# Performance work log

Hardware: AMD Instinct MI355X
Metric: run time of the kernel (lower is better)

The kernel has to match this reference:

```python
import jax, jax.numpy as jnp
import numpy as np

H = 2048
Q_RANK = 256
SCALE = float(np.sqrt(Q_RANK))


def setup_inputs() -> dict:
    key = jax.random.key(0)
    k_x, k_s, k_a, k_o, k_b = jax.random.split(key, 5)
    B, L = 4, 4096
    x = jax.random.normal(k_x, (B, L, H), dtype=jnp.float32)
    # nn.Linear(H, q_rank, bias=False): weight [q_rank, H]; y = x @ W.T -> store transposed [H, q_rank]
    Ws = jax.random.normal(k_s, (H, Q_RANK), dtype=jnp.float32) / np.sqrt(H)
    Wa = jax.random.normal(k_a, (H, Q_RANK), dtype=jnp.float32) / np.sqrt(H)
    Wo = jax.random.normal(k_o, (H, H), dtype=jnp.float32) / np.sqrt(H)
    bo = jax.random.normal(k_b, (H,), dtype=jnp.float32) * 0.01
    return {"x": x, "Ws": Ws, "Wa": Wa, "Wo": Wo, "bo": bo}


def reference(x, Ws, Wa, Wo, bo):
    # x: [B, L, H]
    B, L, _ = x.shape
    state = jnp.einsum('blh,hr->blr', x, Ws)   # [B, L, r]
    action = jnp.einsum('blh,hr->blr', x, Wa)  # [B, L, r]
    q_values = jnp.einsum('bir,bjr->bij', state, action) / SCALE  # [B, L, L]
    # causal mask: position i attends to j <= i
    causal = jnp.tril(jnp.ones((L, L), dtype=bool))
    q_values = jnp.where(causal, q_values, -jnp.inf)
    weights = jax.nn.softmax(q_values, axis=-1)  # [B, L, L]
    out = jnp.einsum('bij,bjh->bih', weights, x)  # weights @ x (x acts as V)
    return jnp.einsum('bih,ho->bio', out, Wo.T) + bo  # out_proj: y = out @ Wo_lin.T; Wo stored as [H,H] input-major
```

## Files before the change

kernel.cpp:

```cpp
#include <hip/hip_runtime.h>
#include <hip/hip_bf16.h>
#include <cstdint>
#include <cstddef>

typedef __bf16 bf16_t;
typedef __bf16 bf16x8 __attribute__((ext_vector_type(8)));
typedef __bf16 bf16x4v __attribute__((ext_vector_type(4)));
typedef float f32x4 __attribute__((ext_vector_type(4)));

#define B_SZ 4
#define L_SZ 4096
#define H_SZ 2048
#define R_SZ 256
#define EXP_SC 0.090168440f
#define E2_ELEMS 8912896L
#define E2_BYTES 17825792L

#define GLDS16(gaddr, laddr)                                                    \
  __builtin_amdgcn_global_load_lds(                                             \
      (const __attribute__((address_space(1))) void*)(gaddr),                   \
      (__attribute__((address_space(3))) void*)(laddr), 16, 0, 0)

__device__ __forceinline__ f32x4 mfma16(bf16x8 a, bf16x8 b, f32x4 c) {
  return __builtin_amdgcn_mfma_f32_16x16x32_bf16(a, b, c, 0, 0, 0);
}

__device__ __forceinline__ float rsum16(float v) {
  v += __shfl_xor(v, 1, 16);
  v += __shfl_xor(v, 2, 16);
  v += __shfl_xor(v, 4, 16);
  v += __shfl_xor(v, 8, 16);
  return v;
}

__global__ void cvt_x_kernel(const float* __restrict__ x, bf16_t* __restrict__ xb, int n4) {
  int i = blockIdx.x * blockDim.x + threadIdx.x;
  const int stride = gridDim.x * blockDim.x;
  for (; i < n4; i += stride) {
    float4 v = reinterpret_cast<const float4*>(x)[i];
    bf16x4v o;
    o[0] = (bf16_t)v.x; o[1] = (bf16_t)v.y; o[2] = (bf16_t)v.z; o[3] = (bf16_t)v.w;
    reinterpret_cast<bf16x4v*>(xb)[i] = o;
  }
}

__global__ void cvt_w_kernel(const float* __restrict__ Ws, const float* __restrict__ Wa,
                             const float* __restrict__ Wo,
                             bf16_t* __restrict__ Wst, bf16_t* __restrict__ Wat,
                             bf16_t* __restrict__ Wob, float* __restrict__ lsum) {
  const int tid = blockIdx.x * blockDim.x + threadIdx.x;
  const int stride = gridDim.x * blockDim.x;
  for (int idx = tid; idx < R_SZ * H_SZ; idx += stride) {
    const int rr = idx >> 11;
    const int h  = idx & (H_SZ - 1);
    Wst[idx] = (bf16_t)Ws[h * R_SZ + rr];
    Wat[idx] = (bf16_t)Wa[h * R_SZ + rr];
  }
  for (int idx = tid; idx < H_SZ * H_SZ; idx += stride) {
    Wob[idx] = (bf16_t)Wo[idx];
  }
  for (int idx = tid; idx < B_SZ * L_SZ; idx += stride) lsum[idx] = 0.0f;
}


#define G8_STG(P, REGION, BUFOFF, HALF)                                        \
  GLDS16((P)[0], lds + (REGION) + (BUFOFF) + (HALF)*16384 + ldst0);            \
  GLDS16((P)[1], lds + (REGION) + (BUFOFF) + (HALF)*16384 + ldst1);            \
  (P)[0] += 128; (P)[1] += 128;

#define G8_LDA(MH, BO) {                                                       \
  const char* ap_ = lds + (BO) + (MH)*16384;                                   \
  fa[0][0] = *(const bf16x8*)(ap_ + aOff0);                                    \
  fa[0][1] = *(const bf16x8*)(ap_ + aOff1);                                    \
  fa[1][0] = *(const bf16x8*)(ap_ + 4096 + aOff0);                             \
  fa[1][1] = *(const bf16x8*)(ap_ + 4096 + aOff1);                             \
  fa[2][0] = *(const bf16x8*)(ap_ + 8192 + aOff0);                             \
  fa[2][1] = *(const bf16x8*)(ap_ + 8192 + aOff1);                             \
  fa[3][0] = *(const bf16x8*)(ap_ + 12288 + aOff0);                            \
  fa[3][1] = *(const bf16x8*)(ap_ + 12288 + aOff1); }

#define G8_LDB(NH, BO) {                                                       \
  const char* bp_ = lds + 65536 + (BO) + (NH)*16384;                           \
  fb[NH][0][0] = *(const bf16x8*)(bp_ + bOff0);                                \
  fb[NH][0][1] = *(const bf16x8*)(bp_ + bOff1);                                \
  fb[NH][1][0] = *(const bf16x8*)(bp_ + 8192 + bOff0);                         \
  fb[NH][1][1] = *(const bf16x8*)(bp_ + 8192 + bOff1); }

#define G8_MM1(AM, AN, MF, NH, J)                                              \
  acc[AM][AN] = mfma16(fa[MF][1], fb[NH][J][1],                                \
                 mfma16(fa[MF][0], fb[NH][J][0], acc[AM][AN]))

#define G8_MM(MH, NH)                                                          \
  G8_MM1((MH)*4+0, (NH)*2+0, 0, NH, 0); G8_MM1((MH)*4+0, (NH)*2+1, 0, NH, 1); \
  G8_MM1((MH)*4+1, (NH)*2+0, 1, NH, 0); G8_MM1((MH)*4+1, (NH)*2+1, 1, NH, 1); \
  G8_MM1((MH)*4+2, (NH)*2+0, 2, NH, 0); G8_MM1((MH)*4+2, (NH)*2+1, 2, NH, 1); \
  G8_MM1((MH)*4+3, (NH)*2+0, 3, NH, 0); G8_MM1((MH)*4+3, (NH)*2+1, 3, NH, 1)

#define G8_PHASE(LOADS, STAGES, WAITS, MH, NH)                                 \
  LOADS;                                                                       \
  STAGES;                                                                      \
  __builtin_amdgcn_sched_barrier(0);                                           \
  __builtin_amdgcn_s_barrier();                                                \
  asm volatile("s_waitcnt lgkmcnt(0)" ::: "memory");                           \
  __builtin_amdgcn_sched_barrier(0);                                           \
  __builtin_amdgcn_s_setprio(1);                                               \
  G8_MM(MH, NH);                                                               \
  __builtin_amdgcn_s_setprio(0);                                               \
  WAITS;                                                                       \
  __builtin_amdgcn_sched_barrier(0);                                           \
  __builtin_amdgcn_s_barrier();

__device__ __forceinline__ void gemm8_core(
    const char* Ag, const char* Bg, long aRowB, long bRowB, int NT,
    char* lds, f32x4 (&acc)[8][4])
{
  const int t = threadIdx.x;
  const int l = t & 63;
  const int wid = t >> 6;
  const int wr = wid >> 2;
  const int wc = wid & 3;
  const int l15 = l & 15;
  const int l4 = l >> 4;
  const int swzm = (l15 & 7) << 4;
  const int aOff0 = (wr * 16 + l15) * 128 + ((l4 * 16) ^ swzm);
  const int aOff1 = (wr * 16 + l15) * 128 + ((64 + l4 * 16) ^ swzm);
  const int bOff0 = (wc * 16 + l15) * 128 + ((l4 * 16) ^ swzm);
  const int bOff1 = (wc * 16 + l15) * 128 + ((64 + l4 * 16) ^ swzm);
  const int d0 = t * 16, d1 = t * 16 + 8192;
  const int r0 = d0 >> 7, r1 = d1 >> 7;
  const int s0 = (d0 & 127) ^ ((r0 & 7) << 4);
  const int s1 = (d1 & 127) ^ ((r1 & 7) << 4);
  const char* pA0[2] = { Ag + (long)r0 * aRowB + s0, Ag + (long)r1 * aRowB + s1 };
  const char* pA1[2] = { Ag + (long)(128 + r0) * aRowB + s0, Ag + (long)(128 + r1) * aRowB + s1 };
  const char* pB0[2] = { Bg + (long)r0 * bRowB + s0, Bg + (long)r1 * bRowB + s1 };
  const char* pB1[2] = { Bg + (long)(128 + r0) * bRowB + s0, Bg + (long)(128 + r1) * bRowB + s1 };
  const int ldst0 = wid * 1024, ldst1 = wid * 1024 + 8192;
  bf16x8 fa[4][2], fb[2][2][2];

  G8_STG(pA0, 0, 0, 0);
  G8_STG(pB0, 65536, 0, 0);
  G8_STG(pA1, 0, 0, 1);
  G8_STG(pB1, 65536, 0, 1);
  G8_STG(pA0, 0, 32768, 0);
  G8_STG(pB0, 65536, 32768, 0);
  asm volatile("s_waitcnt vmcnt(4)" ::: "memory");
  __builtin_amdgcn_sched_barrier(0);
  __builtin_amdgcn_s_barrier();

  int bufOff = 0;
  for (int T = 0; T < NT - 2; ++T) {
    const int ob = bufOff ^ 32768;
    G8_PHASE(G8_LDA(0, bufOff) G8_LDB(0, bufOff), G8_STG(pA1, 0, ob, 1), , 0, 0);
    G8_PHASE(G8_LDB(1, bufOff), G8_STG(pB1, 65536, ob, 1), , 0, 1);
    G8_PHASE(G8_LDA(1, bufOff), G8_STG(pA0, 0, bufOff, 0), , 1, 0);
    G8_PHASE(, G8_STG(pB0, 65536, bufOff, 0),
             asm volatile("s_waitcnt vmcnt(4)" ::: "memory"), 1, 1);
    bufOff ^= 32768;
  }
  {
    const int ob = bufOff ^ 32768;
    G8_PHASE(G8_LDA(0, bufOff) G8_LDB(0, bufOff), G8_STG(pA1, 0, ob, 1), , 0, 0);
    G8_PHASE(G8_LDB(1, bufOff), G8_STG(pB1, 65536, ob, 1), , 0, 1);
    G8_PHASE(G8_LDA(1, bufOff), , , 1, 0);
    G8_PHASE(, , asm volatile("s_waitcnt vmcnt(0)" ::: "memory"), 1, 1);
    bufOff ^= 32768;
  }
  {
    G8_PHASE(G8_LDA(0, bufOff) G8_LDB(0, bufOff), , , 0, 0);
    G8_PHASE(G8_LDB(1, bufOff), , , 0, 1);
    G8_PHASE(G8_LDA(1, bufOff), , , 1, 0);
    G8_PHASE(, , , 1, 1);
  }
}

__global__ __launch_bounds__(512) void qk8_kernel(
    const bf16_t* __restrict__ xb, const bf16_t* __restrict__ Wst,
    const bf16_t* __restrict__ Wat, bf16_t* __restrict__ Qb, bf16_t* __restrict__ Kb)
{
  extern __shared__ char lds[];
  const long mBase = (long)blockIdx.x * 256;
  const bf16_t* W = blockIdx.z ? Wat : Wst;
  bf16_t* Cp = blockIdx.z ? Kb : Qb;
  f32x4 acc[8][4] = {};
  gemm8_core((const char*)xb + mBase * (H_SZ * 2), (const char*)W,
             H_SZ * 2, H_SZ * 2, H_SZ / 64, lds, acc);
  const int t = threadIdx.x, l = t & 63, wid = t >> 6;
  const int wr = wid >> 2, wc = wid & 3, l15 = l & 15, l4 = l >> 4;
#pragma unroll
  for (int am = 0; am < 8; ++am) {
#pragma unroll
    for (int an = 0; an < 4; ++an) {
      const long row = mBase + wr * 16 + am * 32 + l4 * 4;
      const int col = wc * 16 + an * 64 + l15;
#pragma unroll
      for (int r = 0; r < 4; ++r)
        Cp[(row + r) * R_SZ + col] = (bf16_t)acc[am][an][r];
    }
  }
}

__global__ __launch_bounds__(512) void vp8_kernel(
    const bf16_t* __restrict__ Wob, const bf16_t* __restrict__ xb, bf16_t* __restrict__ VT)
{
  extern __shared__ char lds[];
  const int f = blockIdx.x;
  const int lg = (f & 7) * 64 + (f >> 3);
  const int xo = lg & 7;
  const int yj = (lg >> 3) & 15;
  const int b  = lg >> 7;
  const long mBase = (long)xo * 256;
  const long nBase = (long)yj * 256;
  f32x4 acc[8][4] = {};
  gemm8_core((const char*)Wob + mBase * (H_SZ * 2),
             (const char*)xb + ((long)b * L_SZ + nBase) * (H_SZ * 2),
             H_SZ * 2, H_SZ * 2, H_SZ / 64, lds, acc);
  bf16_t* Cp = VT + (long)b * H_SZ * L_SZ;
  const int t = threadIdx.x, l = t & 63, wid = t >> 6;
  const int wr = wid >> 2, wc = wid & 3, l15 = l & 15, l4 = l >> 4;
#pragma unroll
  for (int am = 0; am < 8; ++am) {
#pragma unroll
    for (int an = 0; an < 4; ++an) {
      const long row = mBase + wr * 16 + am * 32 + l4 * 4;
      const long col = nBase + wc * 16 + an * 64 + l15;
#pragma unroll
      for (int r = 0; r < 4; ++r)
        Cp[(row + r) * L_SZ + col] = (bf16_t)acc[am][an][r];
    }
  }
}

__global__ __launch_bounds__(512) void ep8_kernel(
    const bf16_t* __restrict__ Qb, const bf16_t* __restrict__ Kb,
    bf16_t* __restrict__ E, float* __restrict__ lsum)
{
  extern __shared__ char lds[];
  const int P = blockIdx.x;
  const int Jp = blockIdx.y;
  if (Jp > P) return;
  const int b = blockIdx.z;
  f32x4 acc[8][4] = {};
  gemm8_core((const char*)Qb + ((long)b * L_SZ + P * 256) * (R_SZ * 2),
             (const char*)Kb + ((long)b * L_SZ + Jp * 256) * (R_SZ * 2),
             R_SZ * 2, R_SZ * 2, R_SZ / 64, lds, acc);
  const int t = threadIdx.x, l = t & 63, wid = t >> 6;
  const int wr = wid >> 2, wc = wid & 3, l15 = l & 15, l4 = l >> 4;
  bf16_t* Ep = E + (long)b * E2_ELEMS + 32768L * P * (P + 1);
  const long ldaE = (long)(P + 1) * 256;
  float* lp = lsum + (long)b * L_SZ + P * 256;
  const bool diag = (Jp == P);
#pragma unroll
  for (int am = 0; am < 8; ++am) {
    const int rowi = wr * 16 + am * 32 + l4 * 4;
#pragma unroll
    for (int r = 0; r < 4; ++r) {
      float s = 0.0f;
#pragma unroll
      for (int an = 0; an < 4; ++an) {
        const int coli = wc * 16 + an * 64 + l15;
        float p = exp2f(acc[am][an][r] * EXP_SC);
        if (diag && coli > rowi + r) p = 0.0f;
        Ep[(long)(rowi + r) * ldaE + Jp * 256 + coli] = (bf16_t)p;
        s += p;
      }
      s = rsum16(s);
      if (l15 == 0) atomicAdd(lp + rowi + r, s);
    }
  }
}

__global__ __launch_bounds__(512) void pv8_kernel(
    const bf16_t* __restrict__ E, const bf16_t* __restrict__ VT,
    const float* __restrict__ lsum, const float* __restrict__ bo,
    float* __restrict__ out)
{
  extern __shared__ char lds[];
  const int f = blockIdx.x;
  const int lg = (f & 7) * 32 + (f >> 3);
  const int yj = lg & 7;
  const int pr = (lg >> 3) & 7;
  const int b  = lg >> 6;
  const int nBase = yj * 256;
  const int t = threadIdx.x, l = t & 63, wid = t >> 6;
  const int wr = wid >> 2, wc = wid & 3, l15 = l & 15, l4 = l >> 4;

#pragma unroll
  for (int s = 0; s < 2; ++s) {
    const int mt = s ? pr : (15 - pr);
    f32x4 acc[8][4] = {};
    const char* Ag = (const char*)E + (long)b * E2_BYTES + 65536L * mt * (mt + 1);
    const char* Bg = (const char*)VT + ((long)b * H_SZ + nBase) * (L_SZ * 2);
    gemm8_core(Ag, Bg, (long)(mt + 1) * 512, L_SZ * 2, (mt + 1) * 4, lds, acc);
#pragma unroll
    for (int am = 0; am < 8; ++am) {
      const long rowG = (long)b * L_SZ + mt * 256 + wr * 16 + am * 32 + l4 * 4;
      float linv[4];
#pragma unroll
      for (int r = 0; r < 4; ++r) linv[r] = 1.0f / lsum[rowG + r];
#pragma unroll
      for (int an = 0; an < 4; ++an) {
        const int col = nBase + wc * 16 + an * 64 + l15;
        const float bias = bo[col];
#pragma unroll
        for (int r = 0; r < 4; ++r)
          out[(rowG + r) * H_SZ + col] = acc[am][an][r] * linv[r] + bias;
      }
    }
  }
}

extern "C" void kernel_launch(void* const* d_in, const int* in_sizes, int n_in,
                              void* d_out, int out_size, void* d_ws, size_t ws_size,
                              hipStream_t stream) {
  const float* x  = (const float*)d_in[0];
  const float* Ws = (const float*)d_in[1];
  const float* Wa = (const float*)d_in[2];
  const float* Wo = (const float*)d_in[3];
  const float* bo = (const float*)d_in[4];
  float* out = (float*)d_out;

  char* ws = (char*)d_ws;
  bf16_t* xb  = (bf16_t*)(ws + 0);
  bf16_t* Wst = (bf16_t*)(ws + 67108864);
  bf16_t* Wat = (bf16_t*)(ws + 68157440);
  bf16_t* Wob = (bf16_t*)(ws + 69206016);
  bf16_t* Qb  = (bf16_t*)(ws + 77594624);
  bf16_t* Kb  = (bf16_t*)(ws + 85983232);
  bf16_t* VT  = (bf16_t*)(ws + 94371840);
  float*  lsum = (float*)(ws + 161480704);
  bf16_t* E   = (bf16_t*)(ws + 0);

  hipFuncSetAttribute((const void*)qk8_kernel, hipFuncAttributeMaxDynamicSharedMemorySize, 131072);
  hipFuncSetAttribute((const void*)vp8_kernel, hipFuncAttributeMaxDynamicSharedMemorySize, 131072);
  hipFuncSetAttribute((const void*)ep8_kernel, hipFuncAttributeMaxDynamicSharedMemorySize, 131072);
  hipFuncSetAttribute((const void*)pv8_kernel, hipFuncAttributeMaxDynamicSharedMemorySize, 131072);

  cvt_x_kernel<<<dim3(2048), dim3(256), 0, stream>>>(x, xb, B_SZ * L_SZ * H_SZ / 4);
  cvt_w_kernel<<<dim3(1024), dim3(256), 0, stream>>>(Ws, Wa, Wo, Wst, Wat, Wob, lsum);
  qk8_kernel<<<dim3(64, 1, 2), dim3(512), 131072, stream>>>(xb, Wst, Wat, Qb, Kb);
  vp8_kernel<<<dim3(512, 1, 1), dim3(512), 131072, stream>>>(Wob, xb, VT);
  ep8_kernel<<<dim3(16, 16, 4), dim3(512), 131072, stream>>>(Qb, Kb, E, lsum);
  pv8_kernel<<<dim3(256, 1, 1), dim3(512), 131072, stream>>>(E, VT, lsum, bo, out);
}
```

Measured before the change: 410.3 us.

## Merge conversion and projection launches, compact causal grid, drop LDS wait

Folds the x and weight conversion kernels into one launch and merges the Q/K projection GEMM with the value projection GEMM into a single 640-block kernel. The score kernel now launches only the 544 lower-triangular tiles and recovers (P, Jp) with a sqrt-based triangular index plus an XCD-aware remap, instead of launching 1024 blocks and exiting half of them. It also removes the explicit lgkmcnt(0) wait and sched barrier after the block barrier in the GEMM phase. This cuts launch count, idle blocks and tail effects. Dropping the wait relies on the compiler inserting the right waits before the LDS reads are consumed.

```diff
diff --git a/kernel.cpp b/kernel.cpp
--- a/kernel.cpp
+++ b/kernel.cpp
@@ -2,6 +2,7 @@
 #include <hip/hip_bf16.h>
 #include <cstdint>
 #include <cstddef>
+#include <cmath>
 
 typedef __bf16 bf16_t;
 typedef __bf16 bf16x8 __attribute__((ext_vector_type(8)));
@@ -33,23 +34,20 @@
   return v;
 }
 
-__global__ void cvt_x_kernel(const float* __restrict__ x, bf16_t* __restrict__ xb, int n4) {
-  int i = blockIdx.x * blockDim.x + threadIdx.x;
+__global__ void conv_kernel(const float* __restrict__ x, const float* __restrict__ Ws,
+                            const float* __restrict__ Wa, const float* __restrict__ Wo,
+                            bf16_t* __restrict__ xb, bf16_t* __restrict__ Wst,
+                            bf16_t* __restrict__ Wat, bf16_t* __restrict__ Wob,
+                            float* __restrict__ lsum) {
+  const int tid = blockIdx.x * blockDim.x + threadIdx.x;
   const int stride = gridDim.x * blockDim.x;
-  for (; i < n4; i += stride) {
+  const int n4 = B_SZ * L_SZ * H_SZ / 4;
+  for (int i = tid; i < n4; i += stride) {
     float4 v = reinterpret_cast<const float4*>(x)[i];
     bf16x4v o;
     o[0] = (bf16_t)v.x; o[1] = (bf16_t)v.y; o[2] = (bf16_t)v.z; o[3] = (bf16_t)v.w;
     reinterpret_cast<bf16x4v*>(xb)[i] = o;
   }
-}
-
-__global__ void cvt_w_kernel(const float* __restrict__ Ws, const float* __restrict__ Wa,
-                             const float* __restrict__ Wo,
-                             bf16_t* __restrict__ Wst, bf16_t* __restrict__ Wat,
-                             bf16_t* __restrict__ Wob, float* __restrict__ lsum) {
-  const int tid = blockIdx.x * blockDim.x + threadIdx.x;
-  const int stride = gridDim.x * blockDim.x;
   for (int idx = tid; idx < R_SZ * H_SZ; idx += stride) {
     const int rr = idx >> 11;
     const int h  = idx & (H_SZ - 1);
@@ -101,8 +99,6 @@
   STAGES;                                                                      \
   __builtin_amdgcn_sched_barrier(0);                                           \
   __builtin_amdgcn_s_barrier();                                                \
-  asm volatile("s_waitcnt lgkmcnt(0)" ::: "memory");                           \
-  __builtin_amdgcn_sched_barrier(0);                                           \
   __builtin_amdgcn_s_setprio(1);                                               \
   G8_MM(MH, NH);                                                               \
   __builtin_amdgcn_s_setprio(0);                                               \
@@ -173,59 +169,57 @@
   }
 }
 
-__global__ __launch_bounds__(512) void qk8_kernel(
-    const bf16_t* __restrict__ xb, const bf16_t* __restrict__ Wst,
-    const bf16_t* __restrict__ Wat, bf16_t* __restrict__ Qb, bf16_t* __restrict__ Kb)
-{
-  extern __shared__ char lds[];
-  const long mBase = (long)blockIdx.x * 256;
-  const bf16_t* W = blockIdx.z ? Wat : Wst;
-  bf16_t* Cp = blockIdx.z ? Kb : Qb;
-  f32x4 acc[8][4] = {};
-  gemm8_core((const char*)xb + mBase * (H_SZ * 2), (const char*)W,
-             H_SZ * 2, H_SZ * 2, H_SZ / 64, lds, acc);
-  const int t = threadIdx.x, l = t & 63, wid = t >> 6;
-  const int wr = wid >> 2, wc = wid & 3, l15 = l & 15, l4 = l >> 4;
-#pragma unroll
-  for (int am = 0; am < 8; ++am) {
-#pragma unroll
-    for (int an = 0; an < 4; ++an) {
-      const long row = mBase + wr * 16 + am * 32 + l4 * 4;
-      const int col = wc * 16 + an * 64 + l15;
-#pragma unroll
-      for (int r = 0; r < 4; ++r)
-        Cp[(row + r) * R_SZ + col] = (bf16_t)acc[am][an][r];
-    }
-  }
-}
-
-__global__ __launch_bounds__(512) void vp8_kernel(
-    const bf16_t* __restrict__ Wob, const bf16_t* __restrict__ xb, bf16_t* __restrict__ VT)
+__global__ __launch_bounds__(512) void vq8_kernel(
+    const bf16_t* __restrict__ Wob, const bf16_t* __restrict__ xb, bf16_t* __restrict__ VT,
+    const bf16_t* __restrict__ Wst, const bf16_t* __restrict__ Wat,
+    bf16_t* __restrict__ Qb, bf16_t* __restrict__ Kb)
 {
   extern __shared__ char lds[];
   const int f = blockIdx.x;
-  const int lg = (f & 7) * 64 + (f >> 3);
-  const int xo = lg & 7;
-  const int yj = (lg >> 3) & 15;
-  const int b  = lg >> 7;
-  const long mBase = (long)xo * 256;
-  const long nBase = (long)yj * 256;
-  f32x4 acc[8][4] = {};
-  gemm8_core((const char*)Wob + mBase * (H_SZ * 2),
-             (const char*)xb + ((long)b * L_SZ + nBase) * (H_SZ * 2),
-             H_SZ * 2, H_SZ * 2, H_SZ / 64, lds, acc);
-  bf16_t* Cp = VT + (long)b * H_SZ * L_SZ;
   const int t = threadIdx.x, l = t & 63, wid = t >> 6;
   const int wr = wid >> 2, wc = wid & 3, l15 = l & 15, l4 = l >> 4;
-#pragma unroll
-  for (int am = 0; am < 8; ++am) {
-#pragma unroll
-    for (int an = 0; an < 4; ++an) {
-      const long row = mBase + wr * 16 + am * 32 + l4 * 4;
-      const long col = nBase + wc * 16 + an * 64 + l15;
-#pragma unroll
-      for (int r = 0; r < 4; ++r)
-        Cp[(row + r) * L_SZ + col] = (bf16_t)acc[am][an][r];
+  if (f < 128) {
+    const int proj = f >> 6;
+    const long mBase = (long)(f & 63) * 256;
+    const bf16_t* W = proj ? Wat : Wst;
+    bf16_t* Cp = proj ? Kb : Qb;
+    f32x4 acc[8][4] = {};
+    gemm8_core((const char*)xb + mBase * (H_SZ * 2), (const char*)W,
+               H_SZ * 2, H_SZ * 2, H_SZ / 64, lds, acc);
+#pragma unroll
+    for (int am = 0; am < 8; ++am) {
+#pragma unroll
+      for (int an = 0; an < 4; ++an) {
+        const long row = mBase + wr * 16 + am * 32 + l4 * 4;
+        const int col = wc * 16 + an * 64 + l15;
+#pragma unroll
+        for (int r = 0; r < 4; ++r)
+          Cp[(row + r) * R_SZ + col] = (bf16_t)acc[am][an][r];
+      }
+    }
+  } else {
+    const int g = f - 128;
+    const int lg = (g & 7) * 64 + (g >> 3);
+    const int xo = lg & 7;
+    const int yj = (lg >> 3) & 15;
+    const int b  = lg >> 7;
+    const long mBase = (long)xo * 256;
+    const long nBase = (long)yj * 256;
+    f32x4 acc[8][4] = {};
+    gemm8_core((const char*)Wob + mBase * (H_SZ * 2),
+               (const char*)xb + ((long)b * L_SZ + nBase) * (H_SZ * 2),
+               H_SZ * 2, H_SZ * 2, H_SZ / 64, lds, acc);
+    bf16_t* Cp = VT + (long)b * H_SZ * L_SZ;
+#pragma unroll
+    for (int am = 0; am < 8; ++am) {
+#pragma unroll
+      for (int an = 0; an < 4; ++an) {
+        const long row = mBase + wr * 16 + am * 32 + l4 * 4;
+        const long col = nBase + wc * 16 + an * 64 + l15;
+#pragma unroll
+        for (int r = 0; r < 4; ++r)
+          Cp[(row + r) * L_SZ + col] = (bf16_t)acc[am][an][r];
+      }
     }
   }
 }
@@ -235,10 +229,15 @@
     bf16_t* __restrict__ E, float* __restrict__ lsum)
 {
   extern __shared__ char lds[];
-  const int P = blockIdx.x;
-  const int Jp = blockIdx.y;
-  if (Jp > P) return;
-  const int b = blockIdx.z;
+  const int f = blockIdx.x;
+  const int lg = (f & 7) * 68 + (f >> 3);
+  const int b = lg / 136;
+  const int t136 = lg - b * 136;
+  int P = (int)((sqrtf((float)(8 * t136 + 1)) - 1.0f) * 0.5f);
+  while ((P + 1) * (P + 2) / 2 <= t136) ++P;
+  while (P * (P + 1) / 2 > t136) --P;
+  const int Jp = t136 - P * (P + 1) / 2;
+
   f32x4 acc[8][4] = {};
   gemm8_core((const char*)Qb + ((long)b * L_SZ + P * 256) * (R_SZ * 2),
              (const char*)Kb + ((long)b * L_SZ + Jp * 256) * (R_SZ * 2),
@@ -330,15 +329,12 @@
   float*  lsum = (float*)(ws + 161480704);
   bf16_t* E   = (bf16_t*)(ws + 0);
 
-  hipFuncSetAttribute((const void*)qk8_kernel, hipFuncAttributeMaxDynamicSharedMemorySize, 131072);
-  hipFuncSetAttribute((const void*)vp8_kernel, hipFuncAttributeMaxDynamicSharedMemorySize, 131072);
+  hipFuncSetAttribute((const void*)vq8_kernel, hipFuncAttributeMaxDynamicSharedMemorySize, 131072);
   hipFuncSetAttribute((const void*)ep8_kernel, hipFuncAttributeMaxDynamicSharedMemorySize, 131072);
   hipFuncSetAttribute((const void*)pv8_kernel, hipFuncAttributeMaxDynamicSharedMemorySize, 131072);
 
-  cvt_x_kernel<<<dim3(2048), dim3(256), 0, stream>>>(x, xb, B_SZ * L_SZ * H_SZ / 4);
-  cvt_w_kernel<<<dim3(1024), dim3(256), 0, stream>>>(Ws, Wa, Wo, Wst, Wat, Wob, lsum);
-  qk8_kernel<<<dim3(64, 1, 2), dim3(512), 131072, stream>>>(xb, Wst, Wat, Qb, Kb);
-  vp8_kernel<<<dim3(512, 1, 1), dim3(512), 131072, stream>>>(Wob, xb, VT);
-  ep8_kernel<<<dim3(16, 16, 4), dim3(512), 131072, stream>>>(Qb, Kb, E, lsum);
-  pv8_kernel<<<dim3(256, 1, 1), dim3(512), 131072, stream>>>(E, VT, lsum, bo, out);
-}
+  conv_kernel<<<dim3(2048), dim3(256), 0, stream>>>(x, Ws, Wa, Wo, xb, Wst, Wat, Wob, lsum);
+  vq8_kernel<<<dim3(640), dim3(512), 131072, stream>>>(Wob, xb, VT, Wst, Wat, Qb, Kb);
+  ep8_kernel<<<dim3(544), dim3(512), 131072, stream>>>(Qb, Kb, E, lsum);
+  pv8_kernel<<<dim3(256), dim3(512), 131072, stream>>>(E, VT, lsum, bo, out);
+}
```

After: 383.9 us. 1.07x faster.
